# Optimization experiments

Measured on AMD Instinct MI355X. Metric: run time of the kernel, lower is better.

## Reference

```python
import jax, jax.numpy as jnp
import numpy as np

DIM1 = 128; DIM3 = 256; SCALE = 8; DEPTH = 12
RADIUS = 4; NUM_LEVELS = 4; WIN = 2 * RADIUS + 1
HID = 324 + DIM1          # 452 GRU hidden channels
CIN = HID + DIM1          # 580 conv input channels
B = 2; IMG_H = 256; IMG_W = 512
H = IMG_H // SCALE; W = IMG_W // SCALE  # 32, 64


def conv2d(x, w, b, pad):
    y = jax.lax.conv_general_dilated(x, w, (1, 1), pad,
                                     dimension_numbers=('NCHW', 'OIHW', 'NCHW'))
    return y + b[None, :, None, None]


def bilinear_sample(img, coords):
    # img: (C, Hc, Wc); coords: (..., 2) = (x, y) pixel coords; zero padding
    # (equivalent to F.grid_sample(..., align_corners=True) in RAFT)
    C, Hc, Wc = img.shape
    x, y = coords[..., 0], coords[..., 1]
    x0 = jnp.floor(x); y0 = jnp.floor(y)
    wx1 = x - x0; wx0 = 1.0 - wx1
    wy1 = y - y0; wy0 = 1.0 - wy1

    def tap(xi, yi, wgt):
        valid = (xi >= 0) & (xi <= Wc - 1) & (yi >= 0) & (yi <= Hc - 1)
        xc = jnp.clip(xi.astype(jnp.int32), 0, Wc - 1)
        yc = jnp.clip(yi.astype(jnp.int32), 0, Hc - 1)
        return img[:, yc, xc] * (wgt * valid)[None]

    return (tap(x0, y0, wx0 * wy0) + tap(x0 + 1.0, y0, wx1 * wy0)
            + tap(x0, y0 + 1.0, wx0 * wy1) + tap(x0 + 1.0, y0 + 1.0, wx1 * wy1))


def corr_lookup(fmap1, fmap2, coords):
    # RAFT CorrBlock: full all-pairs correlation pyramid + (2r+1)^2 window lookup
    Bn, C, Hh, Ww = fmap1.shape
    corr = jnp.einsum('bcn,bcm->bnm',
                      fmap1.reshape(Bn, C, Hh * Ww),
                      fmap2.reshape(Bn, C, Hh * Ww)) / jnp.sqrt(jnp.float32(C))
    pyr = corr.reshape(Bn * Hh * Ww, 1, Hh, Ww)
    d = jnp.arange(-RADIUS, RADIUS + 1, dtype=jnp.float32)
    cx = coords[:, 0].reshape(-1)   # (B*H*W,) x pixel coords
    cy = coords[:, 1].reshape(-1)
    N = Bn * Hh * Ww
    outs = []
    for lvl in range(NUM_LEVELS):
        sx = cx / (2 ** lvl); sy = cy / (2 ** lvl)
        # RAFT quirk: x-offset varies along window dim 0, y-offset along dim 1
        ox = jnp.broadcast_to(sx[:, None, None] + d[None, :, None], (N, WIN, WIN))
        oy = jnp.broadcast_to(sy[:, None, None] + d[None, None, :], (N, WIN, WIN))
        cl = jnp.stack([ox, oy], axis=-1)                 # (N, 9, 9, 2)
        sampled = jax.vmap(bilinear_sample)(pyr, cl)      # (N, 1, 9, 9)
        outs.append(sampled.reshape(Bn, Hh, Ww, -1))
        n, c, hl, wl = pyr.shape
        pyr = pyr.reshape(n, c, hl // 2, 2, wl // 2, 2).mean(axis=(3, 5))  # avg_pool2d(2,2)
    return jnp.concatenate(outs, axis=-1).transpose(0, 3, 1, 2)  # (B, 324, H, W)


def gru_step(h, xin, params):
    wz1, bz1, wr1, br1, wq1, bq1, wz2, bz2, wr2, br2, wq2, bq2 = params
    p15 = ((0, 0), (2, 2)); p51 = ((2, 2), (0, 0))
    hx = jnp.concatenate([h, xin], axis=1)
    z = jax.nn.sigmoid(conv2d(hx, wz1, bz1, p15))
    r = jax.nn.sigmoid(conv2d(hx, wr1, br1, p15))
    q = jnp.tanh(conv2d(jnp.concatenate([r * h, xin], axis=1), wq1, bq1, p15))
    h = (1.0 - z) * h + z * q
    hx = jnp.concatenate([h, xin], axis=1)
    z = jax.nn.sigmoid(conv2d(hx, wz2, bz2, p51))
    r = jax.nn.sigmoid(conv2d(hx, wr2, br2, p51))
    q = jnp.tanh(conv2d(jnp.concatenate([r * h, xin], axis=1), wq2, bq2, p51))
    return (1.0 - z) * h + z * q


def setup_inputs() -> dict:
    key = jax.random.key(0)
    ks = jax.random.split(key, 17)
    w = lambda k, s: jax.random.normal(k, s, dtype=jnp.float32) * 0.02
    return {
        'x': jax.random.normal(ks[0], (B * 2, H, W, 2 * DIM1), dtype=jnp.float32),
        'image1': jax.random.normal(ks[1], (B, 3, IMG_H, IMG_W), dtype=jnp.float32),
        'i_ana': 0,
        'wz1': w(ks[2], (HID, CIN, 1, 5)), 'bz1': w(ks[3], (HID,)),
        'wr1': w(ks[4], (HID, CIN, 1, 5)), 'br1': w(ks[5], (HID,)),
        'wq1': w(ks[6], (HID, CIN, 1, 5)), 'bq1': w(ks[7], (HID,)),
        'wz2': w(ks[8], (HID, CIN, 5, 1)), 'bz2': w(ks[9], (HID,)),
        'wr2': w(ks[10], (HID, CIN, 5, 1)), 'br2': w(ks[11], (HID,)),
        'wq2': w(ks[12], (HID, CIN, 5, 1)), 'bq2': w(ks[13], (HID,)),
        'wc': w(ks[14], (DIM3, HID, 3, 3)), 'bc': w(ks[15], (DIM3,)),
    }


def reference(x, image1, i_ana, wz1, bz1, wr1, br1, wq1, bq1,
              wz2, bz2, wr2, br2, wq2, bq2, wc, bc):
    Bt = image1.shape[0]
    feat = x.reshape(Bt, 2, H, W, 2 * DIM1)
    fmap1 = feat[:, 0].transpose(0, 3, 1, 2)   # (B, 2*dim1, H, W)
    fmap2 = feat[:, 1].transpose(0, 3, 1, 2)
    net = jnp.tanh(fmap1[:, :DIM1])
    inp = jax.nn.relu(fmap1[:, DIM1:])
    # coords_grid: (B, 2, H, W) with channel 0 = x, channel 1 = y
    gx, gy = jnp.meshgrid(jnp.arange(W, dtype=jnp.float32),
                          jnp.arange(H, dtype=jnp.float32), indexing='xy')
    coords = jnp.broadcast_to(jnp.stack([gx, gy], axis=0)[None], (Bt, 2, H, W))
    corr = corr_lookup(fmap1, fmap2, coords)   # (B, 324, H, W)
    net = jnp.concatenate([corr, net], axis=1)  # (B, 452, H, W)
    params = (wz1, bz1, wr1, br1, wq1, bq1, wz2, bz2, wr2, br2, wq2, bq2)
    for _ in range(DEPTH):
        net = gru_step(net, inp, params)
    out = jax.nn.relu(conv2d(net, wc, bc, ((1, 1), (1, 1))))
    b, c, h2, w2 = out.shape
    return out.reshape(b, c, h2 // 2, 2, w2 // 2, 2).mean(axis=(3, 5))  # AvgPool2d(2,2)
```

## Files before the change

kernel.cpp:

```cpp
#include <hip/hip_runtime.h>
#include <hip/hip_bf16.h>
#include <cstdint>

#define DEV static __device__ __forceinline__

typedef short bf16x8 __attribute__((ext_vector_type(8)));
typedef float f32x4 __attribute__((ext_vector_type(4)));

constexpr size_t CORR0_OFF = 0;
constexpr size_t LVL1_OFF  = CORR0_OFF + 33554432ull;
constexpr size_t LVL2_OFF  = LVL1_OFF  + 8388608ull;
constexpr size_t LVL3_OFF  = LVL2_OFF  + 2097152ull;
constexpr size_t F1_OFF    = LVL3_OFF  + 524288ull;
constexpr size_t F2_OFF    = F1_OFF    + 2097152ull;
constexpr size_t INP_OFF   = F2_OFF    + 2097152ull;
constexpr size_t HF_OFF    = INP_OFF   + 1048576ull;
constexpr size_t HB_OFF    = HF_OFF    + 8388608ull;
constexpr size_t RH_OFF    = HB_OFF    + 4194304ull;
constexpr size_t Z_OFF     = RH_OFF    + 4194304ull;
constexpr size_t CP1_OFF   = Z_OFF     + 8388608ull;
constexpr size_t CP2_OFF   = CP1_OFF   + 25165824ull;
constexpr size_t WA1_OFF   = CP2_OFF   + 25165824ull;
constexpr size_t WA2_OFF   = WA1_OFF   + 5242880ull;
constexpr size_t WB1_OFF   = WA2_OFF   + 5242880ull;
constexpr size_t WB2_OFF   = WB1_OFF   + 2621440ull;
constexpr size_t WI1_OFF   = WB2_OFF   + 2621440ull;
constexpr size_t WI2_OFF   = WI1_OFF   + 1966080ull;
constexpr size_t WFIN_OFF  = WI2_OFF   + 1966080ull;
constexpr size_t OP_OFF    = WFIN_OFF  + 2359296ull;
constexpr size_t ZP_OFF    = OP_OFF    + 4194304ull;

DEV unsigned short f2bf(float f) {
  unsigned int u = __float_as_uint(f);
  u += 0x7fffu + ((u >> 16) & 1u);
  return (unsigned short)(u >> 16);
}
DEV float bf2f(unsigned short u) { return __uint_as_float(((unsigned)u) << 16); }

DEV void gload16(const void* src, void* dst) {
  __builtin_amdgcn_global_load_lds(
      (const __attribute__((address_space(1))) void*)src,
      (__attribute__((address_space(3))) void*)dst, 16, 0, 0);
}

__launch_bounds__(256)
__global__ void prep_kernel(const float* __restrict__ x, unsigned short* f1, unsigned short* f2,
                            float* h_f32, unsigned short* h_b16, unsigned short* inp, float* zp) {
  int bx = blockIdx.x;
  int s = bx >> 11, n = bx & 2047, c = (int)threadIdx.x;
  float v = x[((size_t)(s * 2048 + n)) * 256 + c];
  int b = s >> 1;
  unsigned short bv = f2bf(v);
  size_t p = (size_t)b * 2048 + n;
  if (s & 1) {
    f2[p * 256 + c] = bv;
  } else {
    f1[p * 256 + c] = bv;
    if (c < 128) {
      float tv = tanhf(v);
      h_f32[p * 512 + 324 + c] = tv;
      h_b16[p * 512 + 324 + c] = f2bf(tv);
    } else {
      float rv = fmaxf(v, 0.f);
      inp[p * 128 + (c - 128)] = f2bf(rv);
    }
    if (c < 60) { h_f32[p * 512 + 452 + c] = 0.f; h_b16[p * 512 + 452 + c] = 0; }
  }
  if (bx == 0) zp[c] = 0.f;
}

__launch_bounds__(256)
__global__ void wprep_kernel(const float* s0, const float* s1, const float* s2,
                             unsigned short* dst, int TK, int K, int Kvalid, int icOff,
                             int sOC, int sIC) {
  long idx = (long)blockIdx.x * 256 + threadIdx.x;
  int n = (int)(idx / TK);
  int rem = (int)(idx % TK);
  int t = rem / K, k = rem % K;
  int sec = n >> 9, ocl = n & 511;
  const float* sp = (sec == 0) ? s0 : (sec == 1 ? s1 : s2);
  float v = 0.f;
  if (ocl < 452 && k < Kvalid) v = sp[(size_t)ocl * sOC + (size_t)(icOff + k) * sIC + t];
  dst[idx] = f2bf(v);
}

__launch_bounds__(256)
__global__ void pyr_kernel(const float* __restrict__ corr0, float* l1, float* l2, float* l3) {
  __shared__ float s0[2048];
  __shared__ float s1[512];
  __shared__ float s2[128];
  int bn = blockIdx.x, tid = (int)threadIdx.x;
  const float4* src = (const float4*)(corr0 + (size_t)bn * 2048);
  ((float4*)s0)[tid] = src[tid];
  ((float4*)s0)[tid + 256] = src[tid + 256];
  __syncthreads();
  for (int o = tid; o < 512; o += 256) {
    int yy = o >> 5, xx = o & 31;
    float v = 0.25f * (s0[(yy*2)*64 + xx*2] + s0[(yy*2)*64 + xx*2 + 1] +
                       s0[(yy*2+1)*64 + xx*2] + s0[(yy*2+1)*64 + xx*2 + 1]);
    s1[o] = v; l1[(size_t)bn * 512 + o] = v;
  }
  __syncthreads();
  if (tid < 128) {
    int yy = tid >> 4, xx = tid & 15;
    float v = 0.25f * (s1[(yy*2)*32 + xx*2] + s1[(yy*2)*32 + xx*2 + 1] +
                       s1[(yy*2+1)*32 + xx*2] + s1[(yy*2+1)*32 + xx*2 + 1]);
    s2[tid] = v; l2[(size_t)bn * 128 + tid] = v;
  }
  __syncthreads();
  if (tid < 32) {
    int yy = tid >> 3, xx = tid & 7;
    float v = 0.25f * (s2[(yy*2)*16 + xx*2] + s2[(yy*2)*16 + xx*2 + 1] +
                       s2[(yy*2+1)*16 + xx*2] + s2[(yy*2+1)*16 + xx*2 + 1]);
    l3[(size_t)bn * 32 + tid] = v;
  }
}

__launch_bounds__(256)
__global__ void lookup_kernel(const float* __restrict__ corr0, const float* __restrict__ l1,
                              const float* __restrict__ l2, const float* __restrict__ l3,
                              float* h_f32, unsigned short* h_b16) {
  __shared__ float s0[2048];
  __shared__ float s1[512];
  __shared__ float s2[128];
  __shared__ float s3[32];
  int bn = blockIdx.x, tid = (int)threadIdx.x;
  ((float4*)s0)[tid] = ((const float4*)(corr0 + (size_t)bn * 2048))[tid];
  ((float4*)s0)[tid + 256] = ((const float4*)(corr0 + (size_t)bn * 2048))[tid + 256];
  if (tid < 128) ((float4*)s1)[tid] = ((const float4*)(l1 + (size_t)bn * 512))[tid];
  if (tid < 32)  ((float4*)s2)[tid] = ((const float4*)(l2 + (size_t)bn * 128))[tid];
  if (tid < 8)   ((float4*)s3)[tid] = ((const float4*)(l3 + (size_t)bn * 32))[tid];
  __syncthreads();
  int x = bn & 63, y = (bn >> 6) & 31;
  for (int ch = tid; ch < 324; ch += 256) {
    int lvl = ch / 81, w = ch % 81;
    int di = w / 9 - 4, dj = w % 9 - 4;
    const float* sl = (lvl == 0) ? s0 : (lvl == 1) ? s1 : (lvl == 2) ? s2 : s3;
    int wl = 64 >> lvl, hl = 32 >> lvl;
    float sx = (float)x / (float)(1 << lvl) + (float)di;
    float sy = (float)y / (float)(1 << lvl) + (float)dj;
    float fx0 = floorf(sx), fy0 = floorf(sy);
    int x0 = (int)fx0, y0 = (int)fy0;
    float wx1 = sx - fx0, wx0 = 1.f - wx1;
    float wy1 = sy - fy0, wy0 = 1.f - wy1;
    float acc = 0.f;
    if (x0 >= 0 && x0 < wl && y0 >= 0 && y0 < hl)         acc += sl[y0*wl + x0] * wx0 * wy0;
    if (x0+1 >= 0 && x0+1 < wl && y0 >= 0 && y0 < hl)     acc += sl[y0*wl + x0+1] * wx1 * wy0;
    if (x0 >= 0 && x0 < wl && y0+1 >= 0 && y0+1 < hl)     acc += sl[(y0+1)*wl + x0] * wx0 * wy1;
    if (x0+1 >= 0 && x0+1 < wl && y0+1 >= 0 && y0+1 < hl) acc += sl[(y0+1)*wl + x0+1] * wx1 * wy1;
    h_f32[(size_t)bn * 512 + ch] = acc;
    h_b16[(size_t)bn * 512 + ch] = f2bf(acc);
  }
}

constexpr int KN = 0, KH = 1, KV = 2, KF = 3;
constexpr int EC = 0, EP = 1, EA = 2, EB = 3, EF = 4;

struct GArgs {
  const char* A; int AstrB; long AbatchB;
  const char* B; int KelB;  long BbatchB;
  const float* e0; const float* e1; const float* e2;
  const unsigned short* b0;
  float* f0; unsigned short* u0;
  long CbatchE;
  const char* zp;
};

template<int MT, int KIND, int TAPS>
DEV void stage_act(const char* Ab, int AstrB, char* ldsbuf, int t, int ckOff, int p0, const char* zp) {
  #pragma unroll
  for (int it = 0; it < (MT * 8) / 256; ++it) {
    int gi = it * 256 + (int)threadIdx.x;
    int row = gi >> 3, gs = gi & 7;
    int gl = gs ^ (row & 7);
    int p = p0 + row;
    bool valid = true; int sh = 0;
    if constexpr (KIND == KH) { int d = t - 2; int xx = (p & 63) + d; valid = (unsigned)xx < 64u; sh = d; }
    if constexpr (KIND == KV) { int d = t - 2; int yy = ((p >> 6) & 31) + d; valid = (unsigned)yy < 32u; sh = d * 64; }
    if constexpr (KIND == KF) {
      int tq = t / 3; int ty = tq - 1, tx = (t - tq * 3) - 1;
      int xx = (p & 63) + tx; int yy = ((p >> 6) & 31) + ty;
      valid = ((unsigned)xx < 64u) && ((unsigned)yy < 32u); sh = ty * 64 + tx;
    }
    const char* src = valid ? (Ab + (size_t)(p + sh) * (size_t)AstrB + ckOff + gl * 16)
                            : (zp + gl * 16);
    char* dst = ldsbuf + ((size_t)(it * 256 + ((int)threadIdx.x & ~63)) * 16);
    gload16(src, dst);
  }
}

template<int NT, int TAPS>
DEV void stage_w(const char* Bb, int KelB, char* ldsbuf, int t, int ckOff, int n0) {
  #pragma unroll
  for (int it = 0; it < (NT * 8) / 256; ++it) {
    int gi = it * 256 + (int)threadIdx.x;
    int row = gi >> 3, gs = gi & 7;
    int gl = gs ^ (row & 7);
    int n = n0 + row;
    const char* src = Bb + ((size_t)n * TAPS + t) * (size_t)KelB + ckOff + gl * 16;
    char* dst = ldsbuf + ((size_t)(it * 256 + ((int)threadIdx.x & ~63)) * 16);
    gload16(src, dst);
  }
}

template<int Mf, int Nf, int WM, int WN>
DEV void compute_chunk(const char* lA, const char* lB, f32x4 acc[Mf][Nf], int wm, int wn) {
  const int lane = (int)threadIdx.x & 63;
  const int l15 = lane & 15, g = lane >> 4;
  #pragma unroll
  for (int ks = 0; ks < 2; ++ks) {
    bf16x8 a[Mf], b[Nf];
    int q = ks * 4 + g;
    #pragma unroll
    for (int mf = 0; mf < Mf; ++mf) {
      int r = wm * WM + mf * 16 + l15;
      a[mf] = *(const bf16x8*)(lA + r * 128 + ((q ^ (r & 7)) * 16));
    }
    #pragma unroll
    for (int nf = 0; nf < Nf; ++nf) {
      int r = wn * WN + nf * 16 + l15;
      b[nf] = *(const bf16x8*)(lB + r * 128 + ((q ^ (r & 7)) * 16));
    }
    #pragma unroll
    for (int mf = 0; mf < Mf; ++mf)
      #pragma unroll
      for (int nf = 0; nf < Nf; ++nf)
        acc[mf][nf] = __builtin_amdgcn_mfma_f32_16x16x32_bf16(a[mf], b[nf], acc[mf][nf], 0, 0, 0);
  }
}

template<int EPI>
DEV void epilogue_store(const GArgs& g, float v, int p, int ng, int bz) {
  if constexpr (EPI == EC) {
    g.f0[(size_t)bz * (size_t)g.CbatchE + (size_t)p * 2048 + ng] = v * 0.0625f;
  } else if constexpr (EPI == EP) {
    float bias;
    if (ng < 512)       bias = (ng < 452) ? g.e0[ng] : 0.f;
    else if (ng < 1024) bias = (ng - 512 < 452) ? g.e1[ng - 512] : 0.f;
    else                bias = (ng - 1024 < 452) ? g.e2[ng - 1024] : 0.f;
    g.u0[(size_t)p * 1536 + ng] = f2bf(v + bias);
  } else if constexpr (EPI == EA) {
    float pre = v + bf2f(g.b0[(size_t)p * 1536 + ng]);
    float s = 1.f / (1.f + __expf(-pre));
    if (ng < 512) {
      g.f0[(size_t)p * 512 + ng] = s;
    } else {
      int oc = ng - 512;
      float rh = s * g.e1[(size_t)p * 512 + oc];
      g.u0[(size_t)p * 512 + oc] = f2bf(rh);
    }
  } else if constexpr (EPI == EB) {
    float pre = v + bf2f(g.b0[(size_t)p * 1536 + 1024 + ng]);
    float e = __expf(-2.f * fabsf(pre));
    float tt = (1.f - e) / (1.f + e);
    float qv = (pre < 0.f) ? -tt : tt;
    float z = g.e1[(size_t)p * 512 + ng];
    float ho = g.e2[(size_t)p * 512 + ng];
    float hn = (1.f - z) * ho + z * qv;
    g.f0[(size_t)p * 512 + ng] = hn;
    g.u0[(size_t)p * 512 + ng] = f2bf(hn);
  } else {
    float r = fmaxf(v + g.e0[ng], 0.f);
    g.f0[(size_t)p * 256 + ng] = r;
  }
}

template<int MT, int NT, int WSM, int KIND, int EPI, int TAPS, int CPT, int MINB>
__launch_bounds__(256, MINB)
__global__ void kgemm(GArgs g) {
  constexpr int WSN = 4 / WSM;
  constexpr int WM = MT / WSM, WN = NT / WSN, Mf = WM / 16, Nf = WN / 16;
  constexpr int NC = TAPS * CPT;
  constexpr int BUFB = (MT + NT) * 128;
  __shared__ __attribute__((aligned(16))) char lds[2 * BUFB];
  const int p0 = blockIdx.x * MT, n0 = blockIdx.y * NT;
  const int bz = blockIdx.z;
  const char* Ab = g.A + (size_t)bz * (size_t)g.AbatchB;
  const char* Bb = g.B + (size_t)bz * (size_t)g.BbatchB;
  const int wave = (int)threadIdx.x >> 6;
  const int wm = wave / WSN, wn = wave % WSN;
  f32x4 acc[Mf][Nf] = {};

  auto do_stage = [&](int buf, int c) {
    int t = c / CPT, ck = c % CPT;
    char* base = lds + (size_t)buf * BUFB;
    stage_act<MT, KIND, TAPS>(Ab, g.AstrB, base, t, ck * 128, p0, g.zp);
    stage_w<NT, TAPS>(Bb, g.KelB, base + MT * 128, t, ck * 128, n0);
  };

  do_stage(0, 0);
  asm volatile("s_waitcnt vmcnt(0)" ::: "memory");
  __builtin_amdgcn_s_barrier();
  asm volatile("" ::: "memory");

  #pragma unroll 1
  for (int c = 0; c < NC; ++c) {
    int cur = c & 1;
    if (c + 1 < NC) do_stage(cur ^ 1, c + 1);
    const char* base = lds + (size_t)cur * BUFB;
    compute_chunk<Mf, Nf, WM, WN>(base, base + MT * 128, acc, wm, wn);
    asm volatile("s_waitcnt vmcnt(0)" ::: "memory");
    __builtin_amdgcn_s_barrier();
    asm volatile("" ::: "memory");
  }

  const int lane = (int)threadIdx.x & 63;
  const int l15 = lane & 15, gq = lane >> 4;
  #pragma unroll
  for (int mf = 0; mf < Mf; ++mf)
    #pragma unroll
    for (int nf = 0; nf < Nf; ++nf)
      #pragma unroll
      for (int j = 0; j < 4; ++j) {
        int p = p0 + wm * WM + mf * 16 + gq * 4 + j;
        int ng = n0 + wn * WN + nf * 16 + l15;
        epilogue_store<EPI>(g, acc[mf][nf][j], p, ng, bz);
      }
}

template<int MT, int NT, int KIND, int EPI, int MINB>
__launch_bounds__(256, MINB)
__global__ void hgemm(GArgs g) {
  constexpr int TAPS = 5, CPT = 8;
  constexpr int Gsz = (KIND == KH) ? 64 : 32;
  constexpr int G = MT / Gsz;
  constexpr int S = Gsz + 4;
  constexpr int RA = G * S;
  constexpr int ITA = (RA * 8 + 255) / 256;
  constexpr int WM = MT / 2, WN = NT / 2, Mf = WM / 16, Nf = WN / 16;
  __shared__ __attribute__((aligned(16))) char ldsA[2][RA * 128];
  __shared__ __attribute__((aligned(16))) char ldsB[2][NT * 128];

  const int tid = (int)threadIdx.x;
  const int pg = blockIdx.x * MT;
  const int bz = pg >> 11;
  const int q0 = pg & 2047;
  const int bbase = bz << 11;
  const int n0 = blockIdx.y * NT;
  const char* Ab = g.A + (size_t)bbase * (size_t)g.AstrB;
  const int wave = tid >> 6;
  const int wm = wave >> 1, wn = wave & 1;
  const int lane = tid & 63;
  const int l15 = lane & 15, gq = lane >> 4;
  f32x4 acc[Mf][Nf] = {};

  auto stageA = [&](int buf, int ck) {
    #pragma unroll
    for (int it = 0; it < ITA; ++it) {
      int gi = it * 256 + tid;
      if (ITA * 256 > RA * 8 && gi >= RA * 8) continue;
      int sr = gi >> 3, gs = gi & 7;
      int gl = gs ^ (sr & 7);
      int grp = (G == 1) ? 0 : (sr / S);
      int qq = sr - grp * S;
      bool valid = (qq >= 2) && (qq < Gsz + 2);
      int s = q0 + grp * Gsz + (qq - 2);
      int gpos;
      if constexpr (KIND == KH) gpos = s;
      else gpos = ((s & 31) << 6) + (s >> 5);
      const char* src = valid ? (Ab + (size_t)gpos * (size_t)g.AstrB + ck * 128 + gl * 16)
                              : (g.zp + gl * 16);
      gload16(src, &ldsA[buf][(size_t)(it * 256 + (tid & ~63)) * 16]);
    }
  };
  auto stageB = [&](int buf, int t, int ck) {
    stage_w<NT, TAPS>(g.B, g.KelB, &ldsB[buf][0], t, ck * 128, n0);
  };

  auto computeT = [&](const char* lA, const char* lB, int t) {
    #pragma unroll
    for (int ks = 0; ks < 2; ++ks) {
      bf16x8 a[Mf], b[Nf];
      int q = ks * 4 + gq;
      #pragma unroll
      for (int mf = 0; mf < Mf; ++mf) {
        int m = wm * WM + mf * 16 + l15;
        int r = (m / Gsz) * S + (m % Gsz) + t;
        a[mf] = *(const bf16x8*)(lA + r * 128 + ((q ^ (r & 7)) * 16));
      }
      #pragma unroll
      for (int nf = 0; nf < Nf; ++nf) {
        int r = wn * WN + nf * 16 + l15;
        b[nf] = *(const bf16x8*)(lB + r * 128 + ((q ^ (r & 7)) * 16));
      }
      #pragma unroll
      for (int mf = 0; mf < Mf; ++mf)
        #pragma unroll
        for (int nf = 0; nf < Nf; ++nf)
          acc[mf][nf] = __builtin_amdgcn_mfma_f32_16x16x32_bf16(a[mf], b[nf], acc[mf][nf], 0, 0, 0);
    }
  };

  stageA(0, 0);
  stageB(0, 0, 0);
  asm volatile("s_waitcnt vmcnt(0)" ::: "memory");
  __builtin_amdgcn_s_barrier();
  asm volatile("" ::: "memory");

  int jb = 0;
  #pragma unroll 1
  for (int ck = 0; ck < CPT; ++ck) {
    const char* lA = &ldsA[ck & 1][0];
    #pragma unroll
    for (int t = 0; t < TAPS; ++t) {
      if (t + 1 < TAPS) {
        stageB(jb ^ 1, t + 1, ck);
      } else if (ck + 1 < CPT) {
        stageA((ck + 1) & 1, ck + 1);
        stageB(jb ^ 1, 0, ck + 1);
      }
      computeT(lA, &ldsB[jb][0], t);
      asm volatile("s_waitcnt vmcnt(0)" ::: "memory");
      __builtin_amdgcn_s_barrier();
      asm volatile("" ::: "memory");
      jb ^= 1;
    }
  }

  #pragma unroll
  for (int mf = 0; mf < Mf; ++mf)
    #pragma unroll
    for (int nf = 0; nf < Nf; ++nf)
      #pragma unroll
      for (int j = 0; j < 4; ++j) {
        int m = wm * WM + mf * 16 + gq * 4 + j;
        int s = q0 + m;
        int gpos;
        if constexpr (KIND == KH) gpos = s;
        else gpos = ((s & 31) << 6) + (s >> 5);
        int p = bbase + gpos;
        int ng = n0 + wn * WN + nf * 16 + l15;
        epilogue_store<EPI>(g, acc[mf][nf][j], p, ng, 0);
      }
}

__launch_bounds__(256)
__global__ void pool_kernel(const float* __restrict__ op, float* out) {
  int idx = blockIdx.x * 256 + (int)threadIdx.x;
  int xx = idx & 31, yy = (idx >> 5) & 15, oc = (idx >> 9) & 255, b = idx >> 17;
  size_t p00 = (size_t)b * 2048 + (size_t)(yy * 2) * 64 + xx * 2;
  float v = 0.25f * (op[p00 * 256 + oc] + op[(p00 + 1) * 256 + oc] +
                     op[(p00 + 64) * 256 + oc] + op[(p00 + 65) * 256 + oc]);
  out[idx] = v;
}

extern "C" void kernel_launch(void* const* d_in, const int* in_sizes, int n_in,
                              void* d_out, int out_size, void* d_ws, size_t ws_size,
                              hipStream_t stream) {
  (void)in_sizes; (void)n_in; (void)out_size; (void)ws_size;
  const float* x   = (const float*)d_in[0];
  const float* wz1 = (const float*)d_in[3];  const float* bz1 = (const float*)d_in[4];
  const float* wr1 = (const float*)d_in[5];  const float* br1 = (const float*)d_in[6];
  const float* wq1 = (const float*)d_in[7];  const float* bq1 = (const float*)d_in[8];
  const float* wz2 = (const float*)d_in[9];  const float* bz2 = (const float*)d_in[10];
  const float* wr2 = (const float*)d_in[11]; const float* br2 = (const float*)d_in[12];
  const float* wq2 = (const float*)d_in[13]; const float* bq2 = (const float*)d_in[14];
  const float* wc  = (const float*)d_in[15]; const float* bc  = (const float*)d_in[16];

  char* ws = (char*)d_ws;
  float* corr0 = (float*)(ws + CORR0_OFF);
  float* l1    = (float*)(ws + LVL1_OFF);
  float* l2    = (float*)(ws + LVL2_OFF);
  float* l3    = (float*)(ws + LVL3_OFF);
  unsigned short* f1  = (unsigned short*)(ws + F1_OFF);
  unsigned short* f2p = (unsigned short*)(ws + F2_OFF);
  unsigned short* inp = (unsigned short*)(ws + INP_OFF);
  float* h_f32 = (float*)(ws + HF_OFF);
  unsigned short* h_b16 = (unsigned short*)(ws + HB_OFF);
  unsigned short* rh    = (unsigned short*)(ws + RH_OFF);
  float* zbuf  = (float*)(ws + Z_OFF);
  unsigned short* Cp1 = (unsigned short*)(ws + CP1_OFF);
  unsigned short* Cp2 = (unsigned short*)(ws + CP2_OFF);
  unsigned short* wA1 = (unsigned short*)(ws + WA1_OFF);
  unsigned short* wA2 = (unsigned short*)(ws + WA2_OFF);
  unsigned short* wB1 = (unsigned short*)(ws + WB1_OFF);
  unsigned short* wB2 = (unsigned short*)(ws + WB2_OFF);
  unsigned short* wi1 = (unsigned short*)(ws + WI1_OFF);
  unsigned short* wi2 = (unsigned short*)(ws + WI2_OFF);
  unsigned short* wfn = (unsigned short*)(ws + WFIN_OFF);
  float* outpre = (float*)(ws + OP_OFF);
  float* zp     = (float*)(ws + ZP_OFF);

  prep_kernel<<<8192, 256, 0, stream>>>(x, f1, f2p, h_f32, h_b16, inp, zp);

  wprep_kernel<<<(1024*5*512)/256, 256, 0, stream>>>(wz1, wr1, nullptr, wA1, 5*512, 512, 452, 0, 2900, 5);
  wprep_kernel<<<( 512*5*512)/256, 256, 0, stream>>>(wq1, nullptr, nullptr, wB1, 5*512, 512, 452, 0, 2900, 5);
  wprep_kernel<<<(1536*5*128)/256, 256, 0, stream>>>(wz1, wr1, wq1, wi1, 5*128, 128, 128, 452, 2900, 5);
  wprep_kernel<<<(1024*5*512)/256, 256, 0, stream>>>(wz2, wr2, nullptr, wA2, 5*512, 512, 452, 0, 2900, 5);
  wprep_kernel<<<( 512*5*512)/256, 256, 0, stream>>>(wq2, nullptr, nullptr, wB2, 5*512, 512, 452, 0, 2900, 5);
  wprep_kernel<<<(1536*5*128)/256, 256, 0, stream>>>(wz2, wr2, wq2, wi2, 5*128, 128, 128, 452, 2900, 5);
  wprep_kernel<<<( 256*9*512)/256, 256, 0, stream>>>(wc, nullptr, nullptr, wfn, 9*512, 512, 452, 0, 4068, 9);

  {
    GArgs a = {};
    a.A = (const char*)f1;  a.AstrB = 512; a.AbatchB = 2048L * 512;
    a.B = (const char*)f2p; a.KelB = 512;  a.BbatchB = 2048L * 512;
    a.f0 = corr0; a.CbatchE = 2048L * 2048; a.zp = (const char*)zp;
    kgemm<128,128,2,KN,EC,1,4,2><<<dim3(16,16,2), 256, 0, stream>>>(a);
  }
  pyr_kernel<<<4096, 256, 0, stream>>>(corr0, l1, l2, l3);
  lookup_kernel<<<4096, 256, 0, stream>>>(corr0, l1, l2, l3, h_f32, h_b16);

  {
    GArgs a = {};
    a.A = (const char*)inp; a.AstrB = 256; a.B = (const char*)wi1; a.KelB = 256;
    a.e0 = bz1; a.e1 = br1; a.e2 = bq1; a.u0 = Cp1; a.zp = (const char*)zp;
    kgemm<64,128,2,KH,EP,5,2,3><<<dim3(64,12), 256, 0, stream>>>(a);
  }
  {
    GArgs a = {};
    a.A = (const char*)inp; a.AstrB = 256; a.B = (const char*)wi2; a.KelB = 256;
    a.e0 = bz2; a.e1 = br2; a.e2 = bq2; a.u0 = Cp2; a.zp = (const char*)zp;
    kgemm<64,128,2,KV,EP,5,2,3><<<dim3(64,12), 256, 0, stream>>>(a);
  }

  for (int it = 0; it < 12; ++it) {
    {
      GArgs a = {};
      a.A = (const char*)h_b16; a.AstrB = 1024; a.B = (const char*)wA1; a.KelB = 1024;
      a.b0 = Cp1; a.e1 = h_f32; a.f0 = zbuf; a.u0 = rh; a.zp = (const char*)zp;
      hgemm<64,64,KH,EA,4><<<dim3(64,16), 256, 0, stream>>>(a);
    }
    {
      GArgs a = {};
      a.A = (const char*)rh; a.AstrB = 1024; a.B = (const char*)wB1; a.KelB = 1024;
      a.b0 = Cp1; a.e1 = zbuf; a.e2 = h_f32; a.f0 = h_f32; a.u0 = h_b16; a.zp = (const char*)zp;
      hgemm<64,32,KH,EB,4><<<dim3(64,16), 256, 0, stream>>>(a);
    }
    {
      GArgs a = {};
      a.A = (const char*)h_b16; a.AstrB = 1024; a.B = (const char*)wA2; a.KelB = 1024;
      a.b0 = Cp2; a.e1 = h_f32; a.f0 = zbuf; a.u0 = rh; a.zp = (const char*)zp;
      hgemm<64,64,KV,EA,4><<<dim3(64,16), 256, 0, stream>>>(a);
    }
    {
      GArgs a = {};
      a.A = (const char*)rh; a.AstrB = 1024; a.B = (const char*)wB2; a.KelB = 1024;
      a.b0 = Cp2; a.e1 = zbuf; a.e2 = h_f32; a.f0 = h_f32; a.u0 = h_b16; a.zp = (const char*)zp;
      hgemm<64,32,KV,EB,4><<<dim3(64,16), 256, 0, stream>>>(a);
    }
  }

  {
    GArgs a = {};
    a.A = (const char*)h_b16; a.AstrB = 1024; a.B = (const char*)wfn; a.KelB = 1024;
    a.e0 = bc; a.f0 = outpre; a.zp = (const char*)zp;
    kgemm<64,64,2,KF,EF,9,8,2><<<dim3(64,4), 256, 0, stream>>>(a);
  }
  pool_kernel<<<1024, 256, 0, stream>>>(outpre, (float*)d_out);
}
```

Baseline: 1.773 ms.

## Unify tap convolutions into halo-tiled tgemm staging all taps per K-chunk

Replaces the separable-conv hgemm and the per-tap kgemm paths with a single tgemm kernel. Each K-chunk stages the activation tile once, including halo rows (and a 3-row halo for the 3x3 final conv), together with the weights for all taps, then runs every tap from LDS. This removes the repeated per-tap activation reloads and the many per-tap barriers. The cost is single-buffered LDS with an extra barrier per chunk, so loads no longer overlap compute. Tile shapes and grids also change (128x32 for the z/r GEMMs, narrower N tiles with more blocks elsewhere), and kgemm is reduced to the plain correlation GEMM.

```diff
diff --git a/kernel.cpp b/kernel.cpp
--- a/kernel.cpp
+++ b/kernel.cpp
@@ -175,13 +175,6 @@
     int gl = gs ^ (row & 7);
     int p = p0 + row;
     bool valid = true; int sh = 0;
-    if constexpr (KIND == KH) { int d = t - 2; int xx = (p & 63) + d; valid = (unsigned)xx < 64u; sh = d; }
-    if constexpr (KIND == KV) { int d = t - 2; int yy = ((p >> 6) & 31) + d; valid = (unsigned)yy < 32u; sh = d * 64; }
-    if constexpr (KIND == KF) {
-      int tq = t / 3; int ty = tq - 1, tx = (t - tq * 3) - 1;
-      int xx = (p & 63) + tx; int yy = ((p >> 6) & 31) + ty;
-      valid = ((unsigned)xx < 64u) && ((unsigned)yy < 32u); sh = ty * 64 + tx;
-    }
     const char* src = valid ? (Ab + (size_t)(p + sh) * (size_t)AstrB + ckOff + gl * 16)
                             : (zp + gl * 16);
     char* dst = ldsbuf + ((size_t)(it * 256 + ((int)threadIdx.x & ~63)) * 16);
@@ -265,12 +258,11 @@
   }
 }
 
-template<int MT, int NT, int WSM, int KIND, int EPI, int TAPS, int CPT, int MINB>
+template<int MT, int NT, int WSM, int EPI, int CPT, int MINB>
 __launch_bounds__(256, MINB)
 __global__ void kgemm(GArgs g) {
   constexpr int WSN = 4 / WSM;
   constexpr int WM = MT / WSM, WN = NT / WSN, Mf = WM / 16, Nf = WN / 16;
-  constexpr int NC = TAPS * CPT;
   constexpr int BUFB = (MT + NT) * 128;
   __shared__ __attribute__((aligned(16))) char lds[2 * BUFB];
   const int p0 = blockIdx.x * MT, n0 = blockIdx.y * NT;
@@ -282,10 +274,9 @@
   f32x4 acc[Mf][Nf] = {};
 
   auto do_stage = [&](int buf, int c) {
-    int t = c / CPT, ck = c % CPT;
     char* base = lds + (size_t)buf * BUFB;
-    stage_act<MT, KIND, TAPS>(Ab, g.AstrB, base, t, ck * 128, p0, g.zp);
-    stage_w<NT, TAPS>(Bb, g.KelB, base + MT * 128, t, ck * 128, n0);
+    stage_act<MT, KN, 1>(Ab, g.AstrB, base, 0, c * 128, p0, g.zp);
+    stage_w<NT, 1>(Bb, g.KelB, base + MT * 128, 0, c * 128, n0);
   };
 
   do_stage(0, 0);
@@ -294,9 +285,9 @@
   asm volatile("" ::: "memory");
 
   #pragma unroll 1
-  for (int c = 0; c < NC; ++c) {
+  for (int c = 0; c < CPT; ++c) {
     int cur = c & 1;
-    if (c + 1 < NC) do_stage(cur ^ 1, c + 1);
+    if (c + 1 < CPT) do_stage(cur ^ 1, c + 1);
     const char* base = lds + (size_t)cur * BUFB;
     compute_chunk<Mf, Nf, WM, WN>(base, base + MT * 128, acc, wm, wn);
     asm volatile("s_waitcnt vmcnt(0)" ::: "memory");
@@ -318,18 +309,23 @@
       }
 }
 
-template<int MT, int NT, int KIND, int EPI, int MINB>
+template<int MT, int NT, int KIND, int EPI, int TAPS, int CPT, int MINB>
 __launch_bounds__(256, MINB)
-__global__ void hgemm(GArgs g) {
-  constexpr int TAPS = 5, CPT = 8;
-  constexpr int Gsz = (KIND == KH) ? 64 : 32;
-  constexpr int G = MT / Gsz;
-  constexpr int S = Gsz + 4;
-  constexpr int RA = G * S;
-  constexpr int ITA = (RA * 8 + 255) / 256;
-  constexpr int WM = MT / 2, WN = NT / 2, Mf = WM / 16, Nf = WN / 16;
-  __shared__ __attribute__((aligned(16))) char ldsA[2][RA * 128];
-  __shared__ __attribute__((aligned(16))) char ldsB[2][NT * 128];
+__global__ void tgemm(GArgs g) {
+  constexpr int Gsz = (KIND == KV) ? 32 : 64;
+  constexpr int G   = (KIND == KF) ? 3 : MT / Gsz;
+  constexpr int S   = (KIND == KF) ? 66 : Gsz + 4;
+  constexpr int RA  = G * S;
+  constexpr int RAP = (RA + 7) & ~7;
+  constexpr int RB  = TAPS * NT;
+  constexpr int ITA = (RAP * 8 + 255) / 256;
+  constexpr int ITB = (RB * 8 + 255) / 256;
+  constexpr int WSN = (NT >= 32) ? 2 : 1;
+  constexpr int WSM = 4 / WSN;
+  constexpr int WM = MT / WSM, WN = NT / WSN;
+  constexpr int Mf = WM / 16, Nf = WN / 16;
+  __shared__ __attribute__((aligned(16))) char ldsA[RAP * 128];
+  __shared__ __attribute__((aligned(16))) char ldsB[RB * 128];
 
   const int tid = (int)threadIdx.x;
   const int pg = blockIdx.x * MT;
@@ -339,81 +335,95 @@
   const int n0 = blockIdx.y * NT;
   const char* Ab = g.A + (size_t)bbase * (size_t)g.AstrB;
   const int wave = tid >> 6;
-  const int wm = wave >> 1, wn = wave & 1;
+  const int wm = wave / WSN, wn = wave % WSN;
   const int lane = tid & 63;
   const int l15 = lane & 15, gq = lane >> 4;
   f32x4 acc[Mf][Nf] = {};
 
-  auto stageA = [&](int buf, int ck) {
+  auto stageA = [&](int ck) {
     #pragma unroll
     for (int it = 0; it < ITA; ++it) {
       int gi = it * 256 + tid;
-      if (ITA * 256 > RA * 8 && gi >= RA * 8) continue;
+      if (ITA * 256 > RAP * 8 && gi >= RAP * 8) continue;
       int sr = gi >> 3, gs = gi & 7;
       int gl = gs ^ (sr & 7);
-      int grp = (G == 1) ? 0 : (sr / S);
-      int qq = sr - grp * S;
-      bool valid = (qq >= 2) && (qq < Gsz + 2);
-      int s = q0 + grp * Gsz + (qq - 2);
-      int gpos;
-      if constexpr (KIND == KH) gpos = s;
-      else gpos = ((s & 31) << 6) + (s >> 5);
+      bool valid; int gpos;
+      if constexpr (KIND == KF) {
+        int grp = sr / 66, qq = sr - grp * 66;
+        int y = (q0 >> 6) + grp - 1, x = qq - 1;
+        valid = (sr < RA) && (qq >= 1) && (qq < 65) && ((unsigned)y < 32u);
+        gpos = (y << 6) + x;
+      } else {
+        int grp = (G == 1) ? 0 : (sr / S);
+        int qq = sr - grp * S;
+        valid = (sr < RA) && (qq >= 2) && (qq < Gsz + 2);
+        int s = q0 + grp * Gsz + (qq - 2);
+        if constexpr (KIND == KH) gpos = s;
+        else gpos = ((s & 31) << 6) + (s >> 5);
+      }
       const char* src = valid ? (Ab + (size_t)gpos * (size_t)g.AstrB + ck * 128 + gl * 16)
                               : (g.zp + gl * 16);
-      gload16(src, &ldsA[buf][(size_t)(it * 256 + (tid & ~63)) * 16]);
+      gload16(src, &ldsA[(size_t)(it * 256 + (tid & ~63)) * 16]);
     }
   };
-  auto stageB = [&](int buf, int t, int ck) {
-    stage_w<NT, TAPS>(g.B, g.KelB, &ldsB[buf][0], t, ck * 128, n0);
+  auto stageBf = [&](int ck) {
+    #pragma unroll
+    for (int it = 0; it < ITB; ++it) {
+      int gi = it * 256 + tid;
+      if (ITB * 256 > RB * 8 && gi >= RB * 8) continue;
+      int rb = gi >> 3, gs = gi & 7;
+      int gl = gs ^ (rb & 7);
+      int t = rb / NT, nl = rb - t * NT;
+      const char* src = g.B + ((size_t)(n0 + nl) * TAPS + t) * (size_t)g.KelB + ck * 128 + gl * 16;
+      gload16(src, &ldsB[(size_t)(it * 256 + (tid & ~63)) * 16]);
+    }
   };
 
-  auto computeT = [&](const char* lA, const char* lB, int t) {
-    #pragma unroll
-    for (int ks = 0; ks < 2; ++ks) {
-      bf16x8 a[Mf], b[Nf];
-      int q = ks * 4 + gq;
+  auto computeC = [&]() {
+    #pragma unroll
+    for (int t = 0; t < TAPS; ++t) {
       #pragma unroll
-      for (int mf = 0; mf < Mf; ++mf) {
-        int m = wm * WM + mf * 16 + l15;
-        int r = (m / Gsz) * S + (m % Gsz) + t;
-        a[mf] = *(const bf16x8*)(lA + r * 128 + ((q ^ (r & 7)) * 16));
+      for (int ks = 0; ks < 2; ++ks) {
+        int q = ks * 4 + gq;
+        bf16x8 a[Mf], b[Nf];
+        #pragma unroll
+        for (int mf = 0; mf < Mf; ++mf) {
+          int m = wm * WM + mf * 16 + l15;
+          int r;
+          if constexpr (KIND == KF) r = (t / 3) * 66 + (m & 63) + (t % 3);
+          else r = (m / Gsz) * S + (m % Gsz) + t;
+          a[mf] = *(const bf16x8*)(&ldsA[r * 128 + ((q ^ (r & 7)) * 16)]);
+        }
+        #pragma unroll
+        for (int nf = 0; nf < Nf; ++nf) {
+          int rb = t * NT + wn * WN + nf * 16 + l15;
+          b[nf] = *(const bf16x8*)(&ldsB[rb * 128 + ((q ^ (rb & 7)) * 16)]);
+        }
+        #pragma unroll
+        for (int mf = 0; mf < Mf; ++mf)
+          #pragma unroll
+          for (int nf = 0; nf < Nf; ++nf)
+            acc[mf][nf] = __builtin_amdgcn_mfma_f32_16x16x32_bf16(a[mf], b[nf], acc[mf][nf], 0, 0, 0);
       }
-      #pragma unroll
-      for (int nf = 0; nf < Nf; ++nf) {
-        int r = wn * WN + nf * 16 + l15;
-        b[nf] = *(const bf16x8*)(lB + r * 128 + ((q ^ (r & 7)) * 16));
-      }
-      #pragma unroll
-      for (int mf = 0; mf < Mf; ++mf)
-        #pragma unroll
-        for (int nf = 0; nf < Nf; ++nf)
-          acc[mf][nf] = __builtin_amdgcn_mfma_f32_16x16x32_bf16(a[mf], b[nf], acc[mf][nf], 0, 0, 0);
     }
   };
 
-  stageA(0, 0);
-  stageB(0, 0, 0);
+  stageA(0); stageBf(0);
   asm volatile("s_waitcnt vmcnt(0)" ::: "memory");
   __builtin_amdgcn_s_barrier();
   asm volatile("" ::: "memory");
 
-  int jb = 0;
   #pragma unroll 1
   for (int ck = 0; ck < CPT; ++ck) {
-    const char* lA = &ldsA[ck & 1][0];
-    #pragma unroll
-    for (int t = 0; t < TAPS; ++t) {
-      if (t + 1 < TAPS) {
-        stageB(jb ^ 1, t + 1, ck);
-      } else if (ck + 1 < CPT) {
-        stageA((ck + 1) & 1, ck + 1);
-        stageB(jb ^ 1, 0, ck + 1);
-      }
-      computeT(lA, &ldsB[jb][0], t);
+    computeC();
+    if (ck + 1 < CPT) {
+      asm volatile("" ::: "memory");
+      __builtin_amdgcn_s_barrier();
+      asm volatile("" ::: "memory");
+      stageA(ck + 1); stageBf(ck + 1);
       asm volatile("s_waitcnt vmcnt(0)" ::: "memory");
       __builtin_amdgcn_s_barrier();
       asm volatile("" ::: "memory");
-      jb ^= 1;
     }
   }
 
@@ -426,8 +436,8 @@
         int m = wm * WM + mf * 16 + gq * 4 + j;
         int s = q0 + m;
         int gpos;
-        if constexpr (KIND == KH) gpos = s;
-        else gpos = ((s & 31) << 6) + (s >> 5);
+        if constexpr (KIND == KV) gpos = ((s & 31) << 6) + (s >> 5);
+        else gpos = s;
         int p = bbase + gpos;
         int ng = n0 + wn * WN + nf * 16 + l15;
         epilogue_store<EPI>(g, acc[mf][nf][j], p, ng, 0);
@@ -496,7 +506,7 @@
     a.A = (const char*)f1;  a.AstrB = 512; a.AbatchB = 2048L * 512;
     a.B = (const char*)f2p; a.KelB = 512;  a.BbatchB = 2048L * 512;
     a.f0 = corr0; a.CbatchE = 2048L * 2048; a.zp = (const char*)zp;
-    kgemm<128,128,2,KN,EC,1,4,2><<<dim3(16,16,2), 256, 0, stream>>>(a);
+    kgemm<128,128,2,EC,4,2><<<dim3(16,16,2), 256, 0, stream>>>(a);
   }
   pyr_kernel<<<4096, 256, 0, stream>>>(corr0, l1, l2, l3);
   lookup_kernel<<<4096, 256, 0, stream>>>(corr0, l1, l2, l3, h_f32, h_b16);
@@ -505,13 +515,13 @@
     GArgs a = {};
     a.A = (const char*)inp; a.AstrB = 256; a.B = (const char*)wi1; a.KelB = 256;
     a.e0 = bz1; a.e1 = br1; a.e2 = bq1; a.u0 = Cp1; a.zp = (const char*)zp;
-    kgemm<64,128,2,KH,EP,5,2,3><<<dim3(64,12), 256, 0, stream>>>(a);
+    tgemm<64,32,KH,EP,5,2,4><<<dim3(64,48), 256, 0, stream>>>(a);
   }
   {
     GArgs a = {};
     a.A = (const char*)inp; a.AstrB = 256; a.B = (const char*)wi2; a.KelB = 256;
     a.e0 = bz2; a.e1 = br2; a.e2 = bq2; a.u0 = Cp2; a.zp = (const char*)zp;
-    kgemm<64,128,2,KV,EP,5,2,3><<<dim3(64,12), 256, 0, stream>>>(a);
+    tgemm<64,32,KV,EP,5,2,4><<<dim3(64,48), 256, 0, stream>>>(a);
   }
 
   for (int it = 0; it < 12; ++it) {
@@ -519,25 +529,25 @@
       GArgs a = {};
       a.A = (const char*)h_b16; a.AstrB = 1024; a.B = (const char*)wA1; a.KelB = 1024;
       a.b0 = Cp1; a.e1 = h_f32; a.f0 = zbuf; a.u0 = rh; a.zp = (const char*)zp;
-      hgemm<64,64,KH,EA,4><<<dim3(64,16), 256, 0, stream>>>(a);
+      tgemm<128,32,KH,EA,5,8,4><<<dim3(32,32), 256, 0, stream>>>(a);
     }
     {
       GArgs a = {};
       a.A = (const char*)rh; a.AstrB = 1024; a.B = (const char*)wB1; a.KelB = 1024;
       a.b0 = Cp1; a.e1 = zbuf; a.e2 = h_f32; a.f0 = h_f32; a.u0 = h_b16; a.zp = (const char*)zp;
-      hgemm<64,32,KH,EB,4><<<dim3(64,16), 256, 0, stream>>>(a);
+      tgemm<64,32,KH,EB,5,8,4><<<dim3(64,16), 256, 0, stream>>>(a);
     }
     {
       GArgs a = {};
       a.A = (const char*)h_b16; a.AstrB = 1024; a.B = (const char*)wA2; a.KelB = 1024;
       a.b0 = Cp2; a.e1 = h_f32; a.f0 = zbuf; a.u0 = rh; a.zp = (const char*)zp;
-      hgemm<64,64,KV,EA,4><<<dim3(64,16), 256, 0, stream>>>(a);
+      tgemm<128,32,KV,EA,5,8,4><<<dim3(32,32), 256, 0, stream>>>(a);
     }
     {
       GArgs a = {};
       a.A = (const char*)rh; a.AstrB = 1024; a.B = (const char*)wB2; a.KelB = 1024;
       a.b0 = Cp2; a.e1 = zbuf; a.e2 = h_f32; a.f0 = h_f32; a.u0 = h_b16; a.zp = (const char*)zp;
-      hgemm<64,32,KV,EB,4><<<dim3(64,16), 256, 0, stream>>>(a);
+      tgemm<64,32,KV,EB,5,8,4><<<dim3(64,16), 256, 0, stream>>>(a);
     }
   }
 
@@ -545,7 +555,7 @@
     GArgs a = {};
     a.A = (const char*)h_b16; a.AstrB = 1024; a.B = (const char*)wfn; a.KelB = 1024;
     a.e0 = bc; a.f0 = outpre; a.zp = (const char*)zp;
-    kgemm<64,64,2,KF,EF,9,8,2><<<dim3(64,4), 256, 0, stream>>>(a);
+    tgemm<64,16,KF,EF,9,8,3><<<dim3(64,16), 256, 0, stream>>>(a);
   }
   pool_kernel<<<1024, 256, 0, stream>>>(outpre, (float*)d_out);
 }
```

Result: faster. 1.556 ms (-12.2%).
